# Performance work log

Hardware: AMD Instinct MI355X
Metric: run time of the kernel (lower is better)

The kernel has to match this reference:

```python
import jax, jax.numpy as jnp
import numpy as np

N_NODES = 100000
N_EDGES = 1600000
D = 128  # in_feats = n_hidden = out_feats


def _linear_params(key, d_in, d_out):
    kw, kb = jax.random.split(key)
    scale = 1.0 / np.sqrt(d_in)
    W = jax.random.uniform(kw, (d_in, d_out), jnp.float32, -scale, scale)
    b = jax.random.uniform(kb, (d_out,), jnp.float32, -scale, scale)
    return W, b


def setup_inputs() -> dict:
    key = jax.random.key(0)
    keys = jax.random.split(key, 8)
    x = jax.random.normal(keys[0], (N_NODES, D), jnp.float32)
    edge_index = jax.random.randint(keys[1], (2, N_EDGES), 0, N_NODES, jnp.int64)
    inp = {"x": x, "edge_index": edge_index}
    for l in range(3):
        W1, b1 = _linear_params(keys[2 + 2 * l], D, D)
        W2, b2 = _linear_params(keys[3 + 2 * l], D, D)
        inp[f"W1_{l}"] = W1
        inp[f"b1_{l}"] = b1
        inp[f"W2_{l}"] = W2
        inp[f"b2_{l}"] = b2
    return inp


def _gin_conv(x, src, dst, W1, b1, W2, b2):
    # GINConv: MLP((1+eps)*x + sum_{j->i} x_j), eps=0
    agg = jax.ops.segment_sum(x[src], dst, num_segments=N_NODES)
    h = agg + x
    h = jnp.maximum(h @ W1 + b1, 0.0)
    return h @ W2 + b2


def reference(x, edge_index, W1_0, b1_0, W2_0, b2_0,
              W1_1, b1_1, W2_1, b2_1, W1_2, b1_2, W2_2, b2_2):
    src, dst = edge_index[0], edge_index[1]
    # layer 0 (loop body): conv -> relu
    x = jnp.maximum(_gin_conv(x, src, dst, W1_0, b1_0, W2_0, b2_0), 0.0)
    # layer 1 (num_layers-2): conv -> relu -> dropout (eval: identity)
    x = jnp.maximum(_gin_conv(x, src, dst, W1_1, b1_1, W2_1, b2_1), 0.0)
    # layer 2 (last): conv -> relu
    x = jnp.maximum(_gin_conv(x, src, dst, W1_2, b1_2, W2_2, b2_2), 0.0)
    return x
```

## Files before the change

### kernel.cpp

```cpp
#include <hip/hip_runtime.h>

#define N_NODES 100000
#define N_EDGES 1600000
#define D 128
#define NBUCK 98
#define CAP 20480
#define PCAP 24576

typedef __attribute__((ext_vector_type(8))) short bf16x8;
typedef __attribute__((ext_vector_type(4))) float f32x4;
typedef unsigned long long u64;

__device__ __forceinline__ float b2f_lo(unsigned int u) {
    return __builtin_bit_cast(float, u << 16);
}
__device__ __forceinline__ float b2f_hi(unsigned int u) {
    return __builtin_bit_cast(float, u & 0xFFFF0000u);
}
__device__ __forceinline__ unsigned short f2b(float f) {
    unsigned int u = __builtin_bit_cast(unsigned int, f);
    u += 0x7FFFu + ((u >> 16) & 1u);
    return (unsigned short)(u >> 16);
}


__global__ __launch_bounds__(256) void prep_kernel(
    const float* __restrict__ x, unsigned short* __restrict__ xb,
    const float* __restrict__ W0, const float* __restrict__ W1_, const float* __restrict__ W2_,
    const float* __restrict__ W3, const float* __restrict__ W4, const float* __restrict__ W5,
    unsigned short* __restrict__ T0, unsigned short* __restrict__ T1_,
    unsigned short* __restrict__ T2_, unsigned short* __restrict__ T3,
    unsigned short* __restrict__ T4, unsigned short* __restrict__ T5,
    uint4* __restrict__ dob4, uint4* __restrict__ xs0) {
    int blk = blockIdx.x;
    if (blk < 384) {
        const float* W;
        unsigned short* T;
        switch (blk >> 6) {
            case 0: W = W0; T = T0; break;
            case 1: W = W1_; T = T1_; break;
            case 2: W = W2_; T = T2_; break;
            case 3: W = W3; T = T3; break;
            case 4: W = W4; T = T4; break;
            default: W = W5; T = T5; break;
        }
        int i = (blk & 63) * 256 + threadIdx.x;
        int k = i >> 7, n = i & 127;
        int nt = n >> 4, mr = n & 15;
        int kc = k >> 5, rem = k & 31, quad = rem >> 3, j = rem & 7;
        T[(nt * 4 + kc) * 512 + quad * 128 + mr * 8 + j] = f2b(W[i]);
    } else if (blk < 12884) {
        int i = (blk - 384) * 256 + threadIdx.x;
        if (i < 3200000) {
            float4 v = ((const float4*)x)[i];
            ushort4 o;
            o.x = f2b(v.x); o.y = f2b(v.y); o.z = f2b(v.z); o.w = f2b(v.w);
            ((ushort4*)xb)[i] = o;
        }
    } else {
        int i = (blk - 12884) * 256 + threadIdx.x;
        uint4 z = {0u, 0u, 0u, 0u};
        if (i < 256) dob4[i] = z;
        if (i < 16) xs0[i] = z;
    }
}


__global__ __launch_bounds__(256) void bin_kernel(const int* __restrict__ src,
                                                  const int* __restrict__ dst,
                                                  int* __restrict__ bcur,
                                                  u64* __restrict__ ebuf) {
    __shared__ int h[NBUCK];
    __shared__ int base[NBUCK];
    int tid = threadIdx.x;
    if (tid < NBUCK) h[tid] = 0;
    __syncthreads();
    int e0 = blockIdx.x * 2048;
    int myd[8], mys[8];
#pragma unroll
    for (int i = 0; i < 8; i++) {
        int e = e0 + tid + i * 256;
        int dv = (e < N_EDGES) ? dst[e] : -1;
        myd[i] = dv;
        mys[i] = (e < N_EDGES) ? src[e] : 0;
        if (dv >= 0) atomicAdd(&h[dv >> 10], 1);
    }
    __syncthreads();
    if (tid < NBUCK) {
        int c = h[tid];
        base[tid] = (c > 0) ? (tid * CAP + atomicAdd(&bcur[tid], c)) : 0;
        h[tid] = 0;
    }
    __syncthreads();
#pragma unroll
    for (int i = 0; i < 8; i++) {
        int dv = myd[i];
        if (dv >= 0) {
            int b = dv >> 10;
            int p = base[b] + atomicAdd(&h[b], 1);
            if (p < (b + 1) * CAP)
                ebuf[p] = ((u64)(unsigned int)dv << 32) | (unsigned int)mys[i];
        }
    }
}

__global__ __launch_bounds__(1024) void bucket_all_kernel(const u64* __restrict__ ebuf,
                                                          const int* __restrict__ bcur,
                                                          int* __restrict__ off,
                                                          int* __restrict__ offe,
                                                          int* __restrict__ csr) {
    __shared__ int hist[1024];
    __shared__ int sc[1024];
    __shared__ int cnt[1024];
    int b = blockIdx.x, tid = threadIdx.x;
    int nE = bcur[b]; if (nE > CAP) nE = CAP;
    int base = b * PCAP;
    const u64* slab = ebuf + (size_t)b * CAP;
    hist[tid] = 0;
    cnt[tid] = 0;
    __syncthreads();
    for (int i = tid; i < nE; i += 1024)
        atomicAdd(&hist[(int)(slab[i] >> 32) & 1023], 1);
    __syncthreads();
    int node = b * 1024 + tid;
    int d = hist[tid];
    int dp = (node < N_NODES) ? ((d + 3) & ~3) : 0;
    sc[tid] = dp;
    __syncthreads();
#pragma unroll
    for (int s = 1; s < 1024; s <<= 1) {
        int t = (tid >= s) ? sc[tid - s] : 0;
        __syncthreads();
        sc[tid] += t;
        __syncthreads();
    }
    int excl = sc[tid] - dp;
    sc[tid] = excl;
    if (node < N_NODES) {
        off[node] = base + excl;
        offe[node] = base + excl + dp;
    }
    __syncthreads();
    for (int i = tid; i < nE; i += 1024) {
        u64 e = slab[i];
        int dd = (int)(e >> 32) & 1023;
        int pos = sc[dd] + atomicAdd(&cnt[dd], 1);
        csr[base + pos] = (int)(e & 0xFFFFFFFFu);
    }
    for (int j = d; j < dp; j++) csr[base + excl + j] = N_NODES;
}


__global__ __launch_bounds__(256) void agg_bf16(const unsigned int* __restrict__ xb,
                                                const int* __restrict__ off,
                                                const int* __restrict__ offe,
                                                const int* __restrict__ csr,
                                                unsigned int* __restrict__ t) {
    int node = blockIdx.x * 4 + (threadIdx.x >> 6);
    int lane = threadIdx.x & 63;
    unsigned int v = xb[(size_t)node * 64 + lane];
    float ax = b2f_lo(v), ay = b2f_hi(v);
    int k = off[node], e = offe[node];
    for (; k + 16 <= e; k += 16) {
        int idx[16];
        unsigned int g[16];
#pragma unroll
        for (int i = 0; i < 16; i++) idx[i] = csr[k + i];
#pragma unroll
        for (int i = 0; i < 16; i++) g[i] = xb[(size_t)idx[i] * 64 + lane];
#pragma unroll
        for (int i = 0; i < 16; i++) { ax += b2f_lo(g[i]); ay += b2f_hi(g[i]); }
    }
    if (k + 8 <= e) {
        int idx[8];
        unsigned int g[8];
#pragma unroll
        for (int i = 0; i < 8; i++) idx[i] = csr[k + i];
#pragma unroll
        for (int i = 0; i < 8; i++) g[i] = xb[(size_t)idx[i] * 64 + lane];
#pragma unroll
        for (int i = 0; i < 8; i++) { ax += b2f_lo(g[i]); ay += b2f_hi(g[i]); }
        k += 8;
    }
    if (k < e) {
        int idx[4];
        unsigned int g[4];
#pragma unroll
        for (int i = 0; i < 4; i++) idx[i] = csr[k + i];
#pragma unroll
        for (int i = 0; i < 4; i++) g[i] = xb[(size_t)idx[i] * 64 + lane];
#pragma unroll
        for (int i = 0; i < 4; i++) { ax += b2f_lo(g[i]); ay += b2f_hi(g[i]); }
    }
    t[(size_t)node * 64 + lane] = (unsigned int)f2b(ax) | ((unsigned int)f2b(ay) << 16);
}


template <bool OUT_F32>
__global__ __launch_bounds__(128) void mlp_mfma(const unsigned short* __restrict__ A,
                                                const unsigned short* __restrict__ W1f,
                                                const float* __restrict__ bias1,
                                                const unsigned short* __restrict__ W2f,
                                                const float* __restrict__ bias2,
                                                void* __restrict__ out) {
    __shared__ char smem[2 * 8704];
    int tid = threadIdx.x;
    int wave = tid >> 6, lane = tid & 63;
    int quad = lane >> 4, mr = lane & 15;
    int m_base = blockIdx.x * 64 + wave * 32;
    int m0 = m_base + mr;       if (m0 >= N_NODES) m0 = N_NODES - 1;
    int m1 = m_base + 16 + mr;  if (m1 >= N_NODES) m1 = N_NODES - 1;

    unsigned short* ust = (unsigned short*)(smem + wave * 8704);

    bf16x8 a0[4], a1[4];
#pragma unroll
    for (int kc = 0; kc < 4; kc++) {
        a0[kc] = *(const bf16x8*)(A + (size_t)m0 * D + kc * 32 + quad * 8);
        a1[kc] = *(const bf16x8*)(A + (size_t)m1 * D + kc * 32 + quad * 8);
    }

    f32x4 acc0[8], acc1[8];
#pragma unroll
    for (int nt = 0; nt < 8; nt++) { acc0[nt] = (f32x4)0.0f; acc1[nt] = (f32x4)0.0f; }
#pragma unroll
    for (int nt = 0; nt < 8; nt++) {
#pragma unroll
        for (int kc = 0; kc < 4; kc++) {
            bf16x8 b = *(const bf16x8*)(W1f + (nt * 4 + kc) * 512 + lane * 8);
            acc0[nt] = __builtin_amdgcn_mfma_f32_16x16x32_bf16(a0[kc], b, acc0[nt], 0, 0, 0);
            acc1[nt] = __builtin_amdgcn_mfma_f32_16x16x32_bf16(a1[kc], b, acc1[nt], 0, 0, 0);
        }
    }
#pragma unroll
    for (int nt = 0; nt < 8; nt++) {
        float bv = bias1[nt * 16 + mr];
#pragma unroll
        for (int r = 0; r < 4; r++) {
            ust[(quad * 4 + r) * 136 + nt * 16 + mr] = f2b(fmaxf(acc0[nt][r] + bv, 0.0f));
            ust[2176 + (quad * 4 + r) * 136 + nt * 16 + mr] = f2b(fmaxf(acc1[nt][r] + bv, 0.0f));
        }
    }

#pragma unroll
    for (int kc = 0; kc < 4; kc++) {
        a0[kc] = *(const bf16x8*)&ust[mr * 136 + kc * 32 + quad * 8];
        a1[kc] = *(const bf16x8*)&ust[2176 + mr * 136 + kc * 32 + quad * 8];
    }
#pragma unroll
    for (int nt = 0; nt < 8; nt++) { acc0[nt] = (f32x4)0.0f; acc1[nt] = (f32x4)0.0f; }
#pragma unroll
    for (int nt = 0; nt < 8; nt++) {
#pragma unroll
        for (int kc = 0; kc < 4; kc++) {
            bf16x8 b = *(const bf16x8*)(W2f + (nt * 4 + kc) * 512 + lane * 8);
            acc0[nt] = __builtin_amdgcn_mfma_f32_16x16x32_bf16(a0[kc], b, acc0[nt], 0, 0, 0);
            acc1[nt] = __builtin_amdgcn_mfma_f32_16x16x32_bf16(a1[kc], b, acc1[nt], 0, 0, 0);
        }
    }

    if (OUT_F32) {
        float* st = (float*)ust;
        const int S = 132;
        float* op = (float*)out;
#pragma unroll
        for (int s = 0; s < 2; s++) {
#pragma unroll
            for (int nt = 0; nt < 8; nt++) {
                float bv = bias2[nt * 16 + mr];
#pragma unroll
                for (int r = 0; r < 4; r++) {
                    float v = s ? acc1[nt][r] : acc0[nt][r];
                    st[(quad * 4 + r) * S + nt * 16 + mr] = fmaxf(v + bv, 0.0f);
                }
            }
#pragma unroll
            for (int it = 0; it < 8; it++) {
                int linear = lane + it * 64;
                int row = linear >> 5, col = (linear & 31) << 2;
                int gm = m_base + s * 16 + row;
                if (gm < N_NODES) {
                    float4 val = *(float4*)&st[row * S + col];
                    *(float4*)(op + (size_t)gm * D + col) = val;
                }
            }
        }
    } else {
        const int S = 136;
        unsigned short* op = (unsigned short*)out;
#pragma unroll
        for (int s = 0; s < 2; s++) {
            unsigned short* st = ust + s * 2176;
#pragma unroll
            for (int nt = 0; nt < 8; nt++) {
                float bv = bias2[nt * 16 + mr];
#pragma unroll
                for (int r = 0; r < 4; r++) {
                    float v = s ? acc1[nt][r] : acc0[nt][r];
                    st[(quad * 4 + r) * S + nt * 16 + mr] = f2b(fmaxf(v + bv, 0.0f));
                }
            }
#pragma unroll
            for (int it = 0; it < 4; it++) {
                int linear = lane + it * 64;
                int row = linear >> 4, col = (linear & 15) << 3;
                int gm = m_base + s * 16 + row;
                if (gm < N_NODES) {
                    uint4 val = *(uint4*)&st[row * S + col];
                    *(uint4*)(op + (size_t)gm * D + col) = val;
                }
            }
        }
    }
}


extern "C" void kernel_launch(void* const* d_in, const int* in_sizes, int n_in,
                              void* d_out, int out_size, void* d_ws, size_t ws_size,
                              hipStream_t stream) {
    const float* x = (const float*)d_in[0];
    const int* ei = (const int*)d_in[1];
    const int* srcv = ei;
    const int* dstv = ei + N_EDGES;
    const float* W1[3] = {(const float*)d_in[2], (const float*)d_in[6], (const float*)d_in[10]};
    const float* b1[3] = {(const float*)d_in[3], (const float*)d_in[7], (const float*)d_in[11]};
    const float* W2[3] = {(const float*)d_in[4], (const float*)d_in[8], (const float*)d_in[12]};
    const float* b2[3] = {(const float*)d_in[5], (const float*)d_in[9], (const float*)d_in[13]};

    char* ws = (char*)d_ws;
    int* off  = (int*)ws;
    int* offe = (int*)(ws + 400000);
    unsigned short* Wt[6];
    for (int i = 0; i < 6; i++) Wt[i] = (unsigned short*)(ws + 800000 + i * 32768);
    unsigned short* xb = (unsigned short*)(ws + 1048576);
    unsigned short* P  = (unsigned short*)(ws + 26648832);

    char* dob = (char*)d_out;
    int* bcur = (int*)(dob);
    u64* ebuf = (u64*)(dob + 1048576);
    int* csr  = (int*)(dob + 17104896);

    prep_kernel<<<12885, 256, 0, stream>>>(
        x, xb,
        W1[0], W2[0], W1[1], W2[1], W1[2], W2[2],
        Wt[0], Wt[1], Wt[2], Wt[3], Wt[4], Wt[5],
        (uint4*)dob, (uint4*)(xb + (size_t)N_NODES * D));

    bin_kernel<<<782, 256, 0, stream>>>(srcv, dstv, bcur, ebuf);
    bucket_all_kernel<<<NBUCK, 1024, 0, stream>>>(ebuf, bcur, off, offe, csr);

    const int agg_grid = 25000;
    const int mlp_grid = 1563;

    agg_bf16<<<agg_grid, 256, 0, stream>>>((const unsigned int*)xb, off, offe, csr, (unsigned int*)P);
    mlp_mfma<false><<<mlp_grid, 128, 0, stream>>>(P, Wt[0], b1[0], Wt[1], b2[0], xb);
    agg_bf16<<<agg_grid, 256, 0, stream>>>((const unsigned int*)xb, off, offe, csr, (unsigned int*)P);
    mlp_mfma<false><<<mlp_grid, 128, 0, stream>>>(P, Wt[2], b1[1], Wt[3], b2[1], xb);
    agg_bf16<<<agg_grid, 256, 0, stream>>>((const unsigned int*)xb, off, offe, csr, (unsigned int*)P);
    mlp_mfma<true><<<mlp_grid, 128, 0, stream>>>(P, Wt[4], b1[2], Wt[5], b2[2], d_out);
}
```

Before: 414.5 us.

## Split bf16 node features into column-group planes for cache-local gather aggregation

Stores the bf16 feature matrix as 8 column-group planes of 16 features each (32 bytes per node), and launches aggregation per (column group, 4-node) block so each wave gathers 8 neighbours in parallel over one plane. The per-node neighbour lists are padded to multiples of 8, and partial sums are reduced with cross-lane shuffles. The MLP kernel reads and writes in the same planar layout. The aim is a smaller working set per pass so gathered rows stay in L2/LLC, at the cost of 32-byte gathers, 8x more blocks that each re-read the CSR indices, and more padded edges.

```diff
diff --git a/kernel.cpp b/kernel.cpp
--- a/kernel.cpp
+++ b/kernel.cpp
@@ -5,7 +5,9 @@
 #define D 128
 #define NBUCK 98
 #define CAP 20480
-#define PCAP 24576
+#define PCAP 28672
+#define RSTRIDE_U32 800008
+#define RSTRIDE_S 1600016
 
 typedef __attribute__((ext_vector_type(8))) short bf16x8;
 typedef __attribute__((ext_vector_type(4))) float f32x4;
@@ -25,13 +27,13 @@
 
 
 __global__ __launch_bounds__(256) void prep_kernel(
-    const float* __restrict__ x, unsigned short* __restrict__ xb,
+    const float* __restrict__ x, unsigned int* __restrict__ xbT,
     const float* __restrict__ W0, const float* __restrict__ W1_, const float* __restrict__ W2_,
     const float* __restrict__ W3, const float* __restrict__ W4, const float* __restrict__ W5,
     unsigned short* __restrict__ T0, unsigned short* __restrict__ T1_,
     unsigned short* __restrict__ T2_, unsigned short* __restrict__ T3,
     unsigned short* __restrict__ T4, unsigned short* __restrict__ T5,
-    uint4* __restrict__ dob4, uint4* __restrict__ xs0) {
+    uint4* __restrict__ dob4) {
     int blk = blockIdx.x;
     if (blk < 384) {
         const float* W;
@@ -53,15 +55,24 @@
         int i = (blk - 384) * 256 + threadIdx.x;
         if (i < 3200000) {
             float4 v = ((const float4*)x)[i];
-            ushort4 o;
-            o.x = f2b(v.x); o.y = f2b(v.y); o.z = f2b(v.z); o.w = f2b(v.w);
-            ((ushort4*)xb)[i] = o;
+            int r = i >> 5;
+            int q = i & 31;
+            int dw = q * 2;
+            int cg = dw >> 3;
+            int cj = dw & 7;
+            uint2 o;
+            o.x = (unsigned int)f2b(v.x) | ((unsigned int)f2b(v.y) << 16);
+            o.y = (unsigned int)f2b(v.z) | ((unsigned int)f2b(v.w) << 16);
+            *(uint2*)(xbT + (size_t)cg * RSTRIDE_U32 + (size_t)r * 8 + cj) = o;
         }
     } else {
         int i = (blk - 12884) * 256 + threadIdx.x;
         uint4 z = {0u, 0u, 0u, 0u};
         if (i < 256) dob4[i] = z;
-        if (i < 16) xs0[i] = z;
+        if (i < 64) {
+            int cg = i >> 3, c = i & 7;
+            xbT[(size_t)cg * RSTRIDE_U32 + (size_t)N_NODES * 8 + c] = 0u;
+        }
     }
 }
 
@@ -124,7 +135,7 @@
     __syncthreads();
     int node = b * 1024 + tid;
     int d = hist[tid];
-    int dp = (node < N_NODES) ? ((d + 3) & ~3) : 0;
+    int dp = (node < N_NODES) ? ((d + 7) & ~7) : 0;
     sc[tid] = dp;
     __syncthreads();
 #pragma unroll
@@ -151,48 +162,42 @@
 }
 
 
-__global__ __launch_bounds__(256) void agg_bf16(const unsigned int* __restrict__ xb,
-                                                const int* __restrict__ off,
-                                                const int* __restrict__ offe,
-                                                const int* __restrict__ csr,
-                                                unsigned int* __restrict__ t) {
-    int node = blockIdx.x * 4 + (threadIdx.x >> 6);
+__global__ __launch_bounds__(256) void agg_cg(const unsigned int* __restrict__ xbT,
+                                              const int* __restrict__ off,
+                                              const int* __restrict__ offe,
+                                              const int* __restrict__ csr,
+                                              unsigned int* __restrict__ tT) {
+    int cg = blockIdx.x & 7;
+    int nb = blockIdx.x >> 3;
+    int wave = threadIdx.x >> 6;
     int lane = threadIdx.x & 63;
-    unsigned int v = xb[(size_t)node * 64 + lane];
-    float ax = b2f_lo(v), ay = b2f_hi(v);
+    int e8 = lane >> 3, c = lane & 7;
+    int node = nb * 4 + wave;
+    const unsigned int* xr = xbT + (size_t)cg * RSTRIDE_U32;
+    unsigned int* tr = tT + (size_t)cg * RSTRIDE_U32;
     int k = off[node], e = offe[node];
+    unsigned int me = xr[(size_t)node * 8 + c];
+    float alo = (e8 == 0) ? b2f_lo(me) : 0.0f;
+    float ahi = (e8 == 0) ? b2f_hi(me) : 0.0f;
     for (; k + 16 <= e; k += 16) {
-        int idx[16];
-        unsigned int g[16];
-#pragma unroll
-        for (int i = 0; i < 16; i++) idx[i] = csr[k + i];
-#pragma unroll
-        for (int i = 0; i < 16; i++) g[i] = xb[(size_t)idx[i] * 64 + lane];
-#pragma unroll
-        for (int i = 0; i < 16; i++) { ax += b2f_lo(g[i]); ay += b2f_hi(g[i]); }
-    }
-    if (k + 8 <= e) {
-        int idx[8];
-        unsigned int g[8];
-#pragma unroll
-        for (int i = 0; i < 8; i++) idx[i] = csr[k + i];
-#pragma unroll
-        for (int i = 0; i < 8; i++) g[i] = xb[(size_t)idx[i] * 64 + lane];
-#pragma unroll
-        for (int i = 0; i < 8; i++) { ax += b2f_lo(g[i]); ay += b2f_hi(g[i]); }
-        k += 8;
+        int i0 = csr[k + e8];
+        int i1 = csr[k + 8 + e8];
+        unsigned int v0 = xr[(size_t)i0 * 8 + c];
+        unsigned int v1 = xr[(size_t)i1 * 8 + c];
+        alo += b2f_lo(v0) + b2f_lo(v1);
+        ahi += b2f_hi(v0) + b2f_hi(v1);
     }
     if (k < e) {
-        int idx[4];
-        unsigned int g[4];
-#pragma unroll
-        for (int i = 0; i < 4; i++) idx[i] = csr[k + i];
-#pragma unroll
-        for (int i = 0; i < 4; i++) g[i] = xb[(size_t)idx[i] * 64 + lane];
-#pragma unroll
-        for (int i = 0; i < 4; i++) { ax += b2f_lo(g[i]); ay += b2f_hi(g[i]); }
-    }
-    t[(size_t)node * 64 + lane] = (unsigned int)f2b(ax) | ((unsigned int)f2b(ay) << 16);
+        int i0 = csr[k + e8];
+        unsigned int v0 = xr[(size_t)i0 * 8 + c];
+        alo += b2f_lo(v0);
+        ahi += b2f_hi(v0);
+    }
+    alo += __shfl_xor(alo, 8);  ahi += __shfl_xor(ahi, 8);
+    alo += __shfl_xor(alo, 16); ahi += __shfl_xor(ahi, 16);
+    alo += __shfl_xor(alo, 32); ahi += __shfl_xor(ahi, 32);
+    if (e8 == 0)
+        tr[(size_t)node * 8 + c] = (unsigned int)f2b(alo) | ((unsigned int)f2b(ahi) << 16);
 }
 
 
@@ -216,8 +221,9 @@
     bf16x8 a0[4], a1[4];
 #pragma unroll
     for (int kc = 0; kc < 4; kc++) {
-        a0[kc] = *(const bf16x8*)(A + (size_t)m0 * D + kc * 32 + quad * 8);
-        a1[kc] = *(const bf16x8*)(A + (size_t)m1 * D + kc * 32 + quad * 8);
+        size_t rb = (size_t)(2 * kc + (quad >> 1)) * RSTRIDE_S + (size_t)((quad & 1) * 8);
+        a0[kc] = *(const bf16x8*)(A + rb + (size_t)m0 * 16);
+        a1[kc] = *(const bf16x8*)(A + rb + (size_t)m1 * 16);
     }
 
     f32x4 acc0[8], acc1[8];
@@ -303,11 +309,13 @@
 #pragma unroll
             for (int it = 0; it < 4; it++) {
                 int linear = lane + it * 64;
-                int row = linear >> 4, col = (linear & 15) << 3;
+                int row = linear >> 4, colst = (linear & 15) << 3;
                 int gm = m_base + s * 16 + row;
                 if (gm < N_NODES) {
-                    uint4 val = *(uint4*)&st[row * S + col];
-                    *(uint4*)(op + (size_t)gm * D + col) = val;
+                    uint4 val = *(uint4*)&st[row * S + colst];
+                    unsigned short* dp = op + (size_t)(colst >> 4) * RSTRIDE_S
+                                       + (size_t)gm * 16 + (colst & 15);
+                    *(uint4*)dp = val;
                 }
             }
         }
@@ -332,8 +340,8 @@
     int* offe = (int*)(ws + 400000);
     unsigned short* Wt[6];
     for (int i = 0; i < 6; i++) Wt[i] = (unsigned short*)(ws + 800000 + i * 32768);
-    unsigned short* xb = (unsigned short*)(ws + 1048576);
-    unsigned short* P  = (unsigned short*)(ws + 26648832);
+    unsigned short* xbT = (unsigned short*)(ws + 1048576);
+    unsigned short* PT  = (unsigned short*)(ws + 26648832);
 
     char* dob = (char*)d_out;
     int* bcur = (int*)(dob);
@@ -341,21 +349,21 @@
     int* csr  = (int*)(dob + 17104896);
 
     prep_kernel<<<12885, 256, 0, stream>>>(
-        x, xb,
+        x, (unsigned int*)xbT,
         W1[0], W2[0], W1[1], W2[1], W1[2], W2[2],
         Wt[0], Wt[1], Wt[2], Wt[3], Wt[4], Wt[5],
-        (uint4*)dob, (uint4*)(xb + (size_t)N_NODES * D));
+        (uint4*)dob);
 
     bin_kernel<<<782, 256, 0, stream>>>(srcv, dstv, bcur, ebuf);
     bucket_all_kernel<<<NBUCK, 1024, 0, stream>>>(ebuf, bcur, off, offe, csr);
 
-    const int agg_grid = 25000;
+    const int agg_grid = 200000;
     const int mlp_grid = 1563;
 
-    agg_bf16<<<agg_grid, 256, 0, stream>>>((const unsigned int*)xb, off, offe, csr, (unsigned int*)P);
-    mlp_mfma<false><<<mlp_grid, 128, 0, stream>>>(P, Wt[0], b1[0], Wt[1], b2[0], xb);
-    agg_bf16<<<agg_grid, 256, 0, stream>>>((const unsigned int*)xb, off, offe, csr, (unsigned int*)P);
-    mlp_mfma<false><<<mlp_grid, 128, 0, stream>>>(P, Wt[2], b1[1], Wt[3], b2[1], xb);
-    agg_bf16<<<agg_grid, 256, 0, stream>>>((const unsigned int*)xb, off, offe, csr, (unsigned int*)P);
-    mlp_mfma<true><<<mlp_grid, 128, 0, stream>>>(P, Wt[4], b1[2], Wt[5], b2[2], d_out);
-}
+    agg_cg<<<agg_grid, 256, 0, stream>>>((const unsigned int*)xbT, off, offe, csr, (unsigned int*)PT);
+    mlp_mfma<false><<<mlp_grid, 128, 0, stream>>>(PT, Wt[0], b1[0], Wt[1], b2[0], xbT);
+    agg_cg<<<agg_grid, 256, 0, stream>>>((const unsigned int*)xbT, off, offe, csr, (unsigned int*)PT);
+    mlp_mfma<false><<<mlp_grid, 128, 0, stream>>>(PT, Wt[2], b1[1], Wt[3], b2[1], xbT);
+    agg_cg<<<agg_grid, 256, 0, stream>>>((const unsigned int*)xbT, off, offe, csr, (unsigned int*)PT);
+    mlp_mfma<true><<<mlp_grid, 128, 0, stream>>>(PT, Wt[4], b1[2], Wt[5], b2[2], d_out);
+}
```

Result: slower. 746.7 us (+80.2%).

## Fuse neighbor aggregation with MLP for first two GIN layers

Applied to the files above, without the earlier changes.

Adds a gin_fused kernel in which each wave aggregates 32 nodes' neighbor features into shared memory, then runs both MFMA matmuls directly on that tile. This removes the write and reread of the intermediate aggregate buffer for layers 0 and 1, and uses ping-pong feature buffers so a layer never overwrites its own input. The trade-off is that each wave now walks its 32 nodes one after another with a much smaller grid (782 blocks versus 25000). That may reduce the latency hiding available for the random gathers. The last layer still uses the separate aggregation and MLP kernels.

```diff
diff --git a/kernel.cpp b/kernel.cpp
--- a/kernel.cpp
+++ b/kernel.cpp
@@ -31,7 +31,7 @@
     unsigned short* __restrict__ T0, unsigned short* __restrict__ T1_,
     unsigned short* __restrict__ T2_, unsigned short* __restrict__ T3,
     unsigned short* __restrict__ T4, unsigned short* __restrict__ T5,
-    uint4* __restrict__ dob4, uint4* __restrict__ xs0) {
+    uint4* __restrict__ dob4, uint4* __restrict__ xs0, uint4* __restrict__ xs1) {
     int blk = blockIdx.x;
     if (blk < 384) {
         const float* W;
@@ -61,7 +61,7 @@
         int i = (blk - 12884) * 256 + threadIdx.x;
         uint4 z = {0u, 0u, 0u, 0u};
         if (i < 256) dob4[i] = z;
-        if (i < 16) xs0[i] = z;
+        if (i < 16) { xs0[i] = z; xs1[i] = z; }
     }
 }
 
@@ -197,6 +197,166 @@
 
 
 template <bool OUT_F32>
+__global__ __launch_bounds__(256) void gin_fused(const unsigned int* __restrict__ xbu,
+                                                 const int* __restrict__ off,
+                                                 const int* __restrict__ offe,
+                                                 const int* __restrict__ csr,
+                                                 const unsigned short* __restrict__ W1f,
+                                                 const float* __restrict__ bias1,
+                                                 const unsigned short* __restrict__ W2f,
+                                                 const float* __restrict__ bias2,
+                                                 void* __restrict__ out) {
+    __shared__ unsigned int smem[4 * 2176];
+    int tid = threadIdx.x;
+    int wave = tid >> 6, lane = tid & 63;
+    int quad = lane >> 4, mr = lane & 15;
+    int m_base = blockIdx.x * 128 + wave * 32;
+    unsigned int* wreg = smem + wave * 2176;
+    unsigned short* ust = (unsigned short*)wreg;
+
+    for (int s = 0; s < 32; s++) {
+        int node = m_base + s;
+        if (node >= N_NODES) node = N_NODES - 1;
+        unsigned int me = xbu[(size_t)node * 64 + lane];
+        float ax = b2f_lo(me), ay = b2f_hi(me);
+        int k = off[node], e = offe[node];
+        for (; k + 16 <= e; k += 16) {
+            int idx[16];
+            unsigned int g[16];
+#pragma unroll
+            for (int i = 0; i < 16; i++) idx[i] = csr[k + i];
+#pragma unroll
+            for (int i = 0; i < 16; i++) g[i] = xbu[(size_t)idx[i] * 64 + lane];
+#pragma unroll
+            for (int i = 0; i < 16; i++) { ax += b2f_lo(g[i]); ay += b2f_hi(g[i]); }
+        }
+        if (k + 8 <= e) {
+            int idx[8];
+            unsigned int g[8];
+#pragma unroll
+            for (int i = 0; i < 8; i++) idx[i] = csr[k + i];
+#pragma unroll
+            for (int i = 0; i < 8; i++) g[i] = xbu[(size_t)idx[i] * 64 + lane];
+#pragma unroll
+            for (int i = 0; i < 8; i++) { ax += b2f_lo(g[i]); ay += b2f_hi(g[i]); }
+            k += 8;
+        }
+        if (k < e) {
+            int idx[4];
+            unsigned int g[4];
+#pragma unroll
+            for (int i = 0; i < 4; i++) idx[i] = csr[k + i];
+#pragma unroll
+            for (int i = 0; i < 4; i++) g[i] = xbu[(size_t)idx[i] * 64 + lane];
+#pragma unroll
+            for (int i = 0; i < 4; i++) { ax += b2f_lo(g[i]); ay += b2f_hi(g[i]); }
+        }
+        wreg[s * 68 + lane] = (unsigned int)f2b(ax) | ((unsigned int)f2b(ay) << 16);
+    }
+
+    bf16x8 a0[4], a1[4];
+#pragma unroll
+    for (int kc = 0; kc < 4; kc++) {
+        a0[kc] = *(const bf16x8*)&ust[mr * 136 + kc * 32 + quad * 8];
+        a1[kc] = *(const bf16x8*)&ust[2176 + mr * 136 + kc * 32 + quad * 8];
+    }
+
+    f32x4 acc0[8], acc1[8];
+#pragma unroll
+    for (int nt = 0; nt < 8; nt++) { acc0[nt] = (f32x4)0.0f; acc1[nt] = (f32x4)0.0f; }
+#pragma unroll
+    for (int nt = 0; nt < 8; nt++) {
+#pragma unroll
+        for (int kc = 0; kc < 4; kc++) {
+            bf16x8 b = *(const bf16x8*)(W1f + (nt * 4 + kc) * 512 + lane * 8);
+            acc0[nt] = __builtin_amdgcn_mfma_f32_16x16x32_bf16(a0[kc], b, acc0[nt], 0, 0, 0);
+            acc1[nt] = __builtin_amdgcn_mfma_f32_16x16x32_bf16(a1[kc], b, acc1[nt], 0, 0, 0);
+        }
+    }
+#pragma unroll
+    for (int nt = 0; nt < 8; nt++) {
+        float bv = bias1[nt * 16 + mr];
+#pragma unroll
+        for (int r = 0; r < 4; r++) {
+            ust[(quad * 4 + r) * 136 + nt * 16 + mr] = f2b(fmaxf(acc0[nt][r] + bv, 0.0f));
+            ust[2176 + (quad * 4 + r) * 136 + nt * 16 + mr] = f2b(fmaxf(acc1[nt][r] + bv, 0.0f));
+        }
+    }
+
+#pragma unroll
+    for (int kc = 0; kc < 4; kc++) {
+        a0[kc] = *(const bf16x8*)&ust[mr * 136 + kc * 32 + quad * 8];
+        a1[kc] = *(const bf16x8*)&ust[2176 + mr * 136 + kc * 32 + quad * 8];
+    }
+#pragma unroll
+    for (int nt = 0; nt < 8; nt++) { acc0[nt] = (f32x4)0.0f; acc1[nt] = (f32x4)0.0f; }
+#pragma unroll
+    for (int nt = 0; nt < 8; nt++) {
+#pragma unroll
+        for (int kc = 0; kc < 4; kc++) {
+            bf16x8 b = *(const bf16x8*)(W2f + (nt * 4 + kc) * 512 + lane * 8);
+            acc0[nt] = __builtin_amdgcn_mfma_f32_16x16x32_bf16(a0[kc], b, acc0[nt], 0, 0, 0);
+            acc1[nt] = __builtin_amdgcn_mfma_f32_16x16x32_bf16(a1[kc], b, acc1[nt], 0, 0, 0);
+        }
+    }
+
+    if (OUT_F32) {
+        float* st = (float*)wreg;
+        const int S = 132;
+        float* op = (float*)out;
+#pragma unroll
+        for (int s = 0; s < 2; s++) {
+#pragma unroll
+            for (int nt = 0; nt < 8; nt++) {
+                float bv = bias2[nt * 16 + mr];
+#pragma unroll
+                for (int r = 0; r < 4; r++) {
+                    float v = s ? acc1[nt][r] : acc0[nt][r];
+                    st[(quad * 4 + r) * S + nt * 16 + mr] = fmaxf(v + bv, 0.0f);
+                }
+            }
+#pragma unroll
+            for (int it = 0; it < 8; it++) {
+                int linear = lane + it * 64;
+                int row = linear >> 5, col = (linear & 31) << 2;
+                int gm = m_base + s * 16 + row;
+                if (gm < N_NODES) {
+                    float4 val = *(float4*)&st[row * S + col];
+                    *(float4*)(op + (size_t)gm * D + col) = val;
+                }
+            }
+        }
+    } else {
+        const int S = 136;
+        unsigned short* op = (unsigned short*)out;
+#pragma unroll
+        for (int s = 0; s < 2; s++) {
+            unsigned short* st = ust + s * 2176;
+#pragma unroll
+            for (int nt = 0; nt < 8; nt++) {
+                float bv = bias2[nt * 16 + mr];
+#pragma unroll
+                for (int r = 0; r < 4; r++) {
+                    float v = s ? acc1[nt][r] : acc0[nt][r];
+                    st[(quad * 4 + r) * S + nt * 16 + mr] = f2b(fmaxf(v + bv, 0.0f));
+                }
+            }
+#pragma unroll
+            for (int it = 0; it < 4; it++) {
+                int linear = lane + it * 64;
+                int row = linear >> 4, col = (linear & 15) << 3;
+                int gm = m_base + s * 16 + row;
+                if (gm < N_NODES) {
+                    uint4 val = *(uint4*)&st[row * S + col];
+                    *(uint4*)(op + (size_t)gm * D + col) = val;
+                }
+            }
+        }
+    }
+}
+
+
+template <bool OUT_F32>
 __global__ __launch_bounds__(128) void mlp_mfma(const unsigned short* __restrict__ A,
                                                 const unsigned short* __restrict__ W1f,
                                                 const float* __restrict__ bias1,
@@ -332,8 +492,8 @@
     int* offe = (int*)(ws + 400000);
     unsigned short* Wt[6];
     for (int i = 0; i < 6; i++) Wt[i] = (unsigned short*)(ws + 800000 + i * 32768);
-    unsigned short* xb = (unsigned short*)(ws + 1048576);
-    unsigned short* P  = (unsigned short*)(ws + 26648832);
+    unsigned short* xb0 = (unsigned short*)(ws + 1048576);
+    unsigned short* xb1 = (unsigned short*)(ws + 26648832);
 
     char* dob = (char*)d_out;
     int* bcur = (int*)(dob);
@@ -341,21 +501,21 @@
     int* csr  = (int*)(dob + 17104896);
 
     prep_kernel<<<12885, 256, 0, stream>>>(
-        x, xb,
+        x, xb0,
         W1[0], W2[0], W1[1], W2[1], W1[2], W2[2],
         Wt[0], Wt[1], Wt[2], Wt[3], Wt[4], Wt[5],
-        (uint4*)dob, (uint4*)(xb + (size_t)N_NODES * D));
+        (uint4*)dob,
+        (uint4*)(xb0 + (size_t)N_NODES * D),
+        (uint4*)(xb1 + (size_t)N_NODES * D));
 
     bin_kernel<<<782, 256, 0, stream>>>(srcv, dstv, bcur, ebuf);
     bucket_all_kernel<<<NBUCK, 1024, 0, stream>>>(ebuf, bcur, off, offe, csr);
 
-    const int agg_grid = 25000;
-    const int mlp_grid = 1563;
-
-    agg_bf16<<<agg_grid, 256, 0, stream>>>((const unsigned int*)xb, off, offe, csr, (unsigned int*)P);
-    mlp_mfma<false><<<mlp_grid, 128, 0, stream>>>(P, Wt[0], b1[0], Wt[1], b2[0], xb);
-    agg_bf16<<<agg_grid, 256, 0, stream>>>((const unsigned int*)xb, off, offe, csr, (unsigned int*)P);
-    mlp_mfma<false><<<mlp_grid, 128, 0, stream>>>(P, Wt[2], b1[1], Wt[3], b2[1], xb);
-    agg_bf16<<<agg_grid, 256, 0, stream>>>((const unsigned int*)xb, off, offe, csr, (unsigned int*)P);
-    mlp_mfma<true><<<mlp_grid, 128, 0, stream>>>(P, Wt[4], b1[2], Wt[5], b2[2], d_out);
-}
+    gin_fused<false><<<782, 256, 0, stream>>>((const unsigned int*)xb0, off, offe, csr,
+                                              Wt[0], b1[0], Wt[1], b2[0], xb1);
+    gin_fused<false><<<782, 256, 0, stream>>>((const unsigned int*)xb1, off, offe, csr,
+                                              Wt[2], b1[1], Wt[3], b2[1], xb0);
+    agg_bf16<<<25000, 256, 0, stream>>>((const unsigned int*)xb0, off, offe, csr,
+                                        (unsigned int*)xb1);
+    mlp_mfma<true><<<1563, 128, 0, stream>>>(xb1, Wt[4], b1[2], Wt[5], b2[2], d_out);
+}
```

Measured after the change: 526.7 us. 1.27x slower.

## Pack edge bin entries to 32 bits and write aggregation output in MFMA fragment layout

Applied to the files above, without the earlier changes.

Edge bin entries now pack the local destination (10 bits) and source (22 bits) into one 32-bit word instead of a 64-bit pair, which halves ebuf traffic in binning and bucketing. The aggregation kernel writes its bf16 result straight into the fragment order the MFMA kernel reads, so each lane's A-operand load becomes a contiguous 16-byte chunk instead of a row-strided gather. In exchange the aggregation stores are scattered, and the MLP tail clamps to the last 32-row block.

```diff
diff --git a/kernel.cpp b/kernel.cpp
--- a/kernel.cpp
+++ b/kernel.cpp
@@ -6,6 +6,7 @@
 #define NBUCK 98
 #define CAP 20480
 #define PCAP 24576
+#define NBLK32 3125
 
 typedef __attribute__((ext_vector_type(8))) short bf16x8;
 typedef __attribute__((ext_vector_type(4))) float f32x4;
@@ -69,7 +70,7 @@
 __global__ __launch_bounds__(256) void bin_kernel(const int* __restrict__ src,
                                                   const int* __restrict__ dst,
                                                   int* __restrict__ bcur,
-                                                  u64* __restrict__ ebuf) {
+                                                  unsigned int* __restrict__ ebuf) {
     __shared__ int h[NBUCK];
     __shared__ int base[NBUCK];
     int tid = threadIdx.x;
@@ -99,12 +100,12 @@
             int b = dv >> 10;
             int p = base[b] + atomicAdd(&h[b], 1);
             if (p < (b + 1) * CAP)
-                ebuf[p] = ((u64)(unsigned int)dv << 32) | (unsigned int)mys[i];
-        }
-    }
-}
-
-__global__ __launch_bounds__(1024) void bucket_all_kernel(const u64* __restrict__ ebuf,
+                ebuf[p] = ((unsigned int)(dv & 1023) << 22) | (unsigned int)mys[i];
+        }
+    }
+}
+
+__global__ __launch_bounds__(1024) void bucket_all_kernel(const unsigned int* __restrict__ ebuf,
                                                           const int* __restrict__ bcur,
                                                           int* __restrict__ off,
                                                           int* __restrict__ offe,
@@ -115,12 +116,12 @@
     int b = blockIdx.x, tid = threadIdx.x;
     int nE = bcur[b]; if (nE > CAP) nE = CAP;
     int base = b * PCAP;
-    const u64* slab = ebuf + (size_t)b * CAP;
+    const unsigned int* slab = ebuf + (size_t)b * CAP;
     hist[tid] = 0;
     cnt[tid] = 0;
     __syncthreads();
     for (int i = tid; i < nE; i += 1024)
-        atomicAdd(&hist[(int)(slab[i] >> 32) & 1023], 1);
+        atomicAdd(&hist[slab[i] >> 22], 1);
     __syncthreads();
     int node = b * 1024 + tid;
     int d = hist[tid];
@@ -142,10 +143,10 @@
     }
     __syncthreads();
     for (int i = tid; i < nE; i += 1024) {
-        u64 e = slab[i];
-        int dd = (int)(e >> 32) & 1023;
+        unsigned int e = slab[i];
+        int dd = e >> 22;
         int pos = sc[dd] + atomicAdd(&cnt[dd], 1);
-        csr[base + pos] = (int)(e & 0xFFFFFFFFu);
+        csr[base + pos] = (int)(e & 0x3FFFFFu);
     }
     for (int j = d; j < dp; j++) csr[base + excl + j] = N_NODES;
 }
@@ -155,7 +156,7 @@
                                                 const int* __restrict__ off,
                                                 const int* __restrict__ offe,
                                                 const int* __restrict__ csr,
-                                                unsigned int* __restrict__ t) {
+                                                unsigned int* __restrict__ Pf) {
     int node = blockIdx.x * 4 + (threadIdx.x >> 6);
     int lane = threadIdx.x & 63;
     unsigned int v = xb[(size_t)node * 64 + lane];
@@ -192,7 +193,11 @@
 #pragma unroll
         for (int i = 0; i < 4; i++) { ax += b2f_lo(g[i]); ay += b2f_hi(g[i]); }
     }
-    t[(size_t)node * 64 + lane] = (unsigned int)f2b(ax) | ((unsigned int)f2b(ay) << 16);
+    unsigned int packed = (unsigned int)f2b(ax) | ((unsigned int)f2b(ay) << 16);
+    int B = node >> 5, sblk = (node >> 4) & 1, mr = node & 15;
+    size_t didx = ((size_t)(B * 8 + sblk * 4 + (lane >> 4)) * 64
+                   + ((lane >> 2) & 3) * 16 + mr) * 4 + (lane & 3);
+    Pf[didx] = packed;
 }
 
 
@@ -208,16 +213,16 @@
     int wave = tid >> 6, lane = tid & 63;
     int quad = lane >> 4, mr = lane & 15;
     int m_base = blockIdx.x * 64 + wave * 32;
-    int m0 = m_base + mr;       if (m0 >= N_NODES) m0 = N_NODES - 1;
-    int m1 = m_base + 16 + mr;  if (m1 >= N_NODES) m1 = N_NODES - 1;
+    int B = blockIdx.x * 2 + wave;
+    if (B > NBLK32 - 1) B = NBLK32 - 1;
 
     unsigned short* ust = (unsigned short*)(smem + wave * 8704);
 
     bf16x8 a0[4], a1[4];
 #pragma unroll
     for (int kc = 0; kc < 4; kc++) {
-        a0[kc] = *(const bf16x8*)(A + (size_t)m0 * D + kc * 32 + quad * 8);
-        a1[kc] = *(const bf16x8*)(A + (size_t)m1 * D + kc * 32 + quad * 8);
+        a0[kc] = *(const bf16x8*)(A + ((size_t)(B * 8 + kc) * 64 + lane) * 8);
+        a1[kc] = *(const bf16x8*)(A + ((size_t)(B * 8 + 4 + kc) * 64 + lane) * 8);
     }
 
     f32x4 acc0[8], acc1[8];
@@ -337,8 +342,8 @@
 
     char* dob = (char*)d_out;
     int* bcur = (int*)(dob);
-    u64* ebuf = (u64*)(dob + 1048576);
-    int* csr  = (int*)(dob + 17104896);
+    unsigned int* ebuf = (unsigned int*)(dob + 1048576);
+    int* csr  = (int*)(dob + 10485760);
 
     prep_kernel<<<12885, 256, 0, stream>>>(
         x, xb,
```

After: 413.4 us. About the same (-0.2%).
